# Performance work log

Hardware: AMD Instinct MI355X
Metric: run time of the kernel (lower is better)

The kernel has to match this reference:

```python
import jax, jax.numpy as jnp
import numpy as np

B, T, C, H = 4, 2048, 1024, 16
HS = C // H          # 64
DFF = 4 * C          # 4096
EPS = 1e-5


def _layernorm(x, g, b):
    mu = jnp.mean(x, axis=-1, keepdims=True)
    var = jnp.mean(jnp.square(x - mu), axis=-1, keepdims=True)
    return (x - mu) * jax.lax.rsqrt(var + EPS) * g + b


def setup_inputs() -> dict:
    key = jax.random.key(0)
    ks = jax.random.split(key, 12)
    s = 0.02
    return {
        "x": jax.random.normal(ks[0], (B, T, C), jnp.float32),
        "Wq": jax.random.normal(ks[1], (H, C, HS), jnp.float32) * s,
        "Wk": jax.random.normal(ks[2], (H, C, HS), jnp.float32) * s,
        "Wv": jax.random.normal(ks[3], (H, C, HS), jnp.float32) * s,
        "Wproj": jax.random.normal(ks[4], (C, C), jnp.float32) * s,
        "bproj": jnp.zeros((C,), jnp.float32),
        "ln1_g": jnp.ones((C,), jnp.float32),
        "ln1_b": jnp.zeros((C,), jnp.float32),
        "ln2_g": jnp.ones((C,), jnp.float32),
        "ln2_b": jnp.zeros((C,), jnp.float32),
        "W1": jax.random.normal(ks[5], (C, DFF), jnp.float32) * s,
        "b1": jnp.zeros((DFF,), jnp.float32),
        "W2": jax.random.normal(ks[6], (DFF, C), jnp.float32) * s,
        "b2": jnp.zeros((C,), jnp.float32),
    }


def reference(x, Wq, Wk, Wv, Wproj, bproj, ln1_g, ln1_b, ln2_g, ln2_b, W1, b1, W2, b2):
    Tn = x.shape[1]
    Cn = x.shape[2]
    # --- self-attention on ln1(x) ---
    h = _layernorm(x, ln1_g, ln1_b)
    q = jnp.einsum('btc,hcd->bhtd', h, Wq)
    k = jnp.einsum('btc,hcd->bhtd', h, Wk)
    v = jnp.einsum('btc,hcd->bhtd', h, Wv)
    # NOTE: original scales by C**-0.5 (full embed dim), not head_size**-0.5
    scores = jnp.einsum('bhtd,bhsd->bhts', q, k) * (Cn ** -0.5)
    mask = jnp.tril(jnp.ones((Tn, Tn), dtype=bool))
    scores = jnp.where(mask, scores, jnp.float32(-jnp.inf))
    att = jax.nn.softmax(scores, axis=-1)
    o = jnp.einsum('bhts,bhsd->bhtd', att, v)          # [B,H,T,HS]
    o = o.transpose(0, 2, 1, 3).reshape(x.shape)       # concat heads -> [B,T,C]
    x = x + o @ Wproj + bproj
    # --- feed-forward on ln2(x) ---
    h2 = _layernorm(x, ln2_g, ln2_b)
    x = x + jax.nn.relu(h2 @ W1 + b1) @ W2 + b2
    return x
```

## Files before the change

kernel.cpp:

```cpp
#include <hip/hip_runtime.h>
#include <hip/hip_bf16.h>
#include <stdint.h>

typedef __attribute__((ext_vector_type(8))) __bf16 bf16x8;
typedef __attribute__((ext_vector_type(4))) __bf16 bf16x4;
typedef __attribute__((ext_vector_type(4))) float f32x4;
typedef __attribute__((ext_vector_type(16))) float f32x16;
typedef __attribute__((ext_vector_type(4))) unsigned int u32x4;

typedef const __attribute__((address_space(1))) void* gas_ptr;
typedef __attribute__((address_space(3))) void* las_ptr;

static __device__ __forceinline__ void gload_lds16(const void* g, void* l) {
  __builtin_amdgcn_global_load_lds((gas_ptr)g, (las_ptr)l, 16, 0, 0);
}

static __device__ __forceinline__ unsigned int cvt_pk(float lo, float hi) {
  unsigned int r;
  asm("v_cvt_pk_bf16_f32 %0, %1, %2" : "=v"(r) : "v"(lo), "v"(hi));
  return r;
}

static __device__ __forceinline__ bf16x8 pack_frag(unsigned int a, unsigned int b,
                                                   unsigned int c, unsigned int d) {
  u32x4 t = {a, b, c, d};
  return __builtin_bit_cast(bf16x8, t);
}

static __device__ __forceinline__ void vm4() {
  asm volatile("s_waitcnt vmcnt(4)" ::: "memory");
}
static __device__ __forceinline__ void phase_bar() {
  asm volatile("" ::: "memory");
  __builtin_amdgcn_s_barrier();
  asm volatile("" ::: "memory");
}

__global__ void transpose_cvt(const float* __restrict__ in, __bf16* __restrict__ out,
                              int R, int S) {
  __shared__ float t[32][33];
  int tx = threadIdx.x, ty = threadIdx.y;
  int r0 = blockIdx.y * 32, s0 = blockIdx.x * 32;
#pragma unroll
  for (int i = 0; i < 4; ++i) {
    int r = r0 + ty + i * 8;
    if (r < R && (s0 + tx) < S) t[ty + i * 8][tx] = in[(size_t)r * S + s0 + tx];
  }
  __syncthreads();
#pragma unroll
  for (int i = 0; i < 4; ++i) {
    int s = s0 + ty + i * 8;
    if (s < S && (r0 + tx) < R) out[(size_t)s * R + r0 + tx] = (__bf16)t[tx][ty + i * 8];
  }
}

__global__ void qkv_repack(const float* __restrict__ Wq, const float* __restrict__ Wk,
                           const float* __restrict__ Wv, __bf16* __restrict__ outT) {
  __shared__ float t[32][33];
  int z = blockIdx.z, sel = z >> 4, h = z & 15;
  const float* in = (sel == 0 ? Wq : sel == 1 ? Wk : Wv) + (size_t)h * 1024 * 64;
  __bf16* out = outT + (size_t)(sel * 1024 + h * 64) * 1024;
  int tx = threadIdx.x, ty = threadIdx.y;
  int r0 = blockIdx.y * 32, s0 = blockIdx.x * 32;
#pragma unroll
  for (int i = 0; i < 4; ++i)
    t[ty + i * 8][tx] = in[(size_t)(r0 + ty + i * 8) * 64 + s0 + tx];
  __syncthreads();
#pragma unroll
  for (int i = 0; i < 4; ++i)
    out[(size_t)(s0 + ty + i * 8) * 1024 + r0 + tx] = (__bf16)t[tx][ty + i * 8];
}

__global__ __launch_bounds__(256) void ln_kernel(const float* __restrict__ x,
                                                 const float* __restrict__ g,
                                                 const float* __restrict__ b,
                                                 __bf16* __restrict__ out) {
  __shared__ float red[8];
  int row = blockIdx.x, tid = threadIdx.x;
  float4 v = ((const float4*)(x + (size_t)row * 1024))[tid];
  float s = v.x + v.y + v.z + v.w;
  float s2 = v.x * v.x + v.y * v.y + v.z * v.z + v.w * v.w;
#pragma unroll
  for (int m = 1; m < 64; m <<= 1) { s += __shfl_xor(s, m); s2 += __shfl_xor(s2, m); }
  if ((tid & 63) == 0) { red[tid >> 6] = s; red[4 + (tid >> 6)] = s2; }
  __syncthreads();
  s = red[0] + red[1] + red[2] + red[3];
  s2 = red[4] + red[5] + red[6] + red[7];
  float mu = s * (1.0f / 1024.0f);
  float var = s2 * (1.0f / 1024.0f) - mu * mu;
  float rs = rsqrtf(var + 1e-5f);
  float4 gg = ((const float4*)g)[tid];
  float4 bb = ((const float4*)b)[tid];
  bf16x4 o4;
  o4[0] = (__bf16)((v.x - mu) * rs * gg.x + bb.x);
  o4[1] = (__bf16)((v.y - mu) * rs * gg.y + bb.y);
  o4[2] = (__bf16)((v.z - mu) * rs * gg.z + bb.z);
  o4[3] = (__bf16)((v.w - mu) * rs * gg.w + bb.w);
  *(bf16x4*)(out + (size_t)row * 1024 + tid * 4) = o4;
}

__global__ __launch_bounds__(256) void add_bias_inplace(float* __restrict__ out,
                                                        const float* __restrict__ bias) {
  int i = blockIdx.x * 256 + threadIdx.x;
  float4 v = ((float4*)out)[i];
  float4 bb = ((const float4*)bias)[i & 255];
  v.x += bb.x; v.y += bb.y; v.z += bb.z; v.w += bb.w;
  ((float4*)out)[i] = v;
}

template <int EPI>
__global__ __launch_bounds__(512) void gemm8p(const __bf16* __restrict__ A,
                                              const __bf16* __restrict__ Bt,
                                              void* __restrict__ Cout,
                                              const float* __restrict__ bias,
                                              const float* __restrict__ resid,
                                              __bf16* __restrict__ q_out,
                                              __bf16* __restrict__ k_out,
                                              __bf16* __restrict__ vt_out,
                                              int M, int N, int K, int NBN) {
  __shared__ __align__(16) char lds[131072];
  const int tid = threadIdx.x;
  const int l = tid & 63, w = tid >> 6;
  const int wm = w >> 2, wn = w & 3;
  const int lr = l & 15, lg = l >> 4;

  int nwg = gridDim.x;
  int cpx = nwg >> 3;
  int orig = blockIdx.x;
  int wgid = (orig & 7) * cpx + (orig >> 3);
  int bn = wgid % NBN, bm = wgid / NBN;
  int n0 = bn * 256, m0 = bm * 256;

  const int Kloop = K / (int)gridDim.z;
  const int NT = Kloop >> 6;
  const size_t K2 = (size_t)K * 2;
  const size_t koff = (size_t)blockIdx.z * Kloop * 2;

  const int srow = tid >> 3, slot = tid & 7;
  const int sswz = (slot ^ (srow & 7)) << 4;
  const char* aA = (const char*)A + (size_t)(m0 + srow) * K2 + koff + sswz;
  const char* aB = (const char*)Bt + (size_t)(n0 + srow) * K2 + koff + sswz;

  auto stageA = [&](char* buf, int half, int kt) {
    char* d = buf + half * 16384 + tid * 16;
    const char* s = aA + (size_t)(half * 128) * K2 + (size_t)kt * 128;
    gload_lds16(s, d);
    gload_lds16(s + (size_t)64 * K2, d + 8192);
  };
  auto stageB = [&](char* buf, int half, int kt) {
    char* d = buf + 32768 + half * 16384 + tid * 16;
    const char* s = aB + (size_t)(half * 128) * K2 + (size_t)kt * 128;
    gload_lds16(s, d);
    gload_lds16(s + (size_t)64 * K2, d + 8192);
  };

  const int arow = (wm * 64 + lr) * 128;
  const int brow = (wn * 32 + lr) * 128;
  const int ck0 = ((lg) ^ (lr & 7)) << 4;
  const int ck1 = ((4 + lg) ^ (lr & 7)) << 4;

  f32x4 acc[8][4];
#pragma unroll
  for (int mi = 0; mi < 8; ++mi)
#pragma unroll
    for (int ni = 0; ni < 4; ++ni)
#pragma unroll
      for (int e = 0; e < 4; ++e) acc[mi][ni][e] = 0.0f;

  bf16x8 af[4][2], bfr[4][2];

  auto ldsA = [&](char* buf, int mh) {
#pragma unroll
    for (int i = 0; i < 4; ++i) {
      const char* p = buf + mh * 16384 + arow + i * 2048;
      af[i][0] = *(const bf16x8*)(p + ck0);
      af[i][1] = *(const bf16x8*)(p + ck1);
    }
  };
  auto ldsB2 = [&](char* buf, int nh) {
#pragma unroll
    for (int j = 0; j < 2; ++j) {
      const char* p = buf + 32768 + nh * 16384 + brow + j * 2048;
      bfr[nh * 2 + j][0] = *(const bf16x8*)(p + ck0);
      bfr[nh * 2 + j][1] = *(const bf16x8*)(p + ck1);
    }
  };
  auto mm = [&](int mh, int nh) {
    __builtin_amdgcn_s_setprio(1);
#pragma unroll
    for (int i = 0; i < 4; ++i)
#pragma unroll
      for (int j = 0; j < 2; ++j) {
        int mi = mh * 4 + i, ni = nh * 2 + j;
        acc[mi][ni] = __builtin_amdgcn_mfma_f32_16x16x32_bf16(af[i][0], bfr[ni][0], acc[mi][ni], 0, 0, 0);
        acc[mi][ni] = __builtin_amdgcn_mfma_f32_16x16x32_bf16(af[i][1], bfr[ni][1], acc[mi][ni], 0, 0, 0);
      }
    __builtin_amdgcn_s_setprio(0);
  };

  {
    char* b0 = lds;
    stageA(b0, 0, 0);
    stageB(b0, 0, 0);
    stageB(b0, 1, 0);
    stageA(b0, 1, 0);
  }

  for (int t = 0; t < NT; ++t) {
    char* cur = lds + ((t & 1) << 16);
    char* nxt = lds + (((t + 1) & 1) << 16);
    int kt = (t + 1 < NT) ? (t + 1) : (NT - 1);
    vm4();
    phase_bar();
    ldsA(cur, 0);
    ldsB2(cur, 0);
    stageA(nxt, 0, kt);
    mm(0, 0);
    vm4();
    phase_bar();
    ldsB2(cur, 1);
    stageB(nxt, 0, kt);
    mm(0, 1);
    vm4();
    phase_bar();
    ldsA(cur, 1);
    stageB(nxt, 1, kt);
    mm(1, 0);
    phase_bar();
    stageA(nxt, 1, kt);
    mm(1, 1);
  }

#pragma unroll
  for (int mi = 0; mi < 8; ++mi) {
    int rowb = m0 + (mi >> 2) * 128 + wm * 64 + (mi & 3) * 16 + lg * 4;
#pragma unroll
    for (int e = 0; e < 4; ++e) {
      int row = rowb + e;
#pragma unroll
      for (int ni = 0; ni < 4; ++ni) {
        int col = n0 + (ni >> 1) * 128 + wn * 32 + (ni & 1) * 16 + lr;
        float v = acc[mi][ni][e];
        size_t idx = (size_t)row * N + col;
        if (EPI == 0) {
          ((__bf16*)Cout)[idx] = (__bf16)v;
        } else if (EPI == 1) {
          ((float*)Cout)[idx] = resid[idx] + v + bias[col];
        } else if (EPI == 2) {
          v += bias[col];
          ((__bf16*)Cout)[idx] = (__bf16)fmaxf(v, 0.0f);
        } else if (EPI == 3) {
          unsafeAtomicAdd(&((float*)Cout)[idx], v);
        } else {
          int b = row >> 11, t = row & 2047;
          int sel = col >> 10, cc = col & 1023, h = cc >> 6, d = cc & 63;
          int bh = b * 16 + h;
          __bf16 val = (__bf16)v;
          if (sel == 0)
            q_out[((size_t)bh * 64 + d) * 2048 + t] = val;
          else if (sel == 1)
            k_out[((size_t)bh * 2048 + t) * 64 + d] = val;
          else
            vt_out[((size_t)bh * 64 + d) * 2048 + t] = val;
        }
      }
    }
  }
}

__global__ __launch_bounds__(256) void attn_kernel3(const __bf16* __restrict__ Qt,
                                                    const __bf16* __restrict__ Kh,
                                                    const __bf16* __restrict__ Vt,
                                                    __bf16* __restrict__ o) {
  __shared__ __align__(16) char Klds[8192];
  __shared__ __align__(16) char Vlds[8192];
  int tid = threadIdx.x;
  int l = tid & 63, w = tid >> 6;
  int lq = l & 31, hi = l >> 5;
  int p = blockIdx.x, bh = blockIdx.y;
  int b = bh >> 4, h = bh & 15;

  const char* Kbase = (const char*)(Kh + (size_t)bh * 2048 * 64);
  const char* Vbase = (const char*)(Vt + (size_t)bh * 64 * 2048);
  const __bf16* Qbase = Qt + (size_t)bh * 64 * 2048;
  __bf16* Obase = o + (size_t)b * 2048 * 1024 + h * 64;

  int srow = tid >> 3;
  int schunk = (tid & 7) * 16;
  int sw0 = (srow & 7) << 4;
  char* kd0 = Klds + tid * 16;
  char* kd1 = Klds + 4096 + tid * 16;
  char* vd0 = Vlds + tid * 16;
  char* vd1 = Vlds + 4096 + tid * 16;
  int swz = (lq & 7) << 4;

  for (int sweep = 0; sweep < 2; ++sweep) {
    int t = (sweep == 0) ? p : 15 - p;
    int qw = t * 128 + w * 32;
    int qglob = qw + lq;

    bf16x8 qb[4];
    const __bf16* qsrc = Qbase + (size_t)(hi * 8) * 2048 + qw + lq;
#pragma unroll
    for (int s = 0; s < 4; ++s)
#pragma unroll
      for (int j = 0; j < 8; ++j)
        qb[s][j] = qsrc[(size_t)(s * 16 + j) * 2048];

    f32x16 oacc0, oacc1;
#pragma unroll
    for (int i = 0; i < 16; ++i) { oacc0[i] = 0.0f; oacc1[i] = 0.0f; }
    float m_q = -3.0e38f, l_q = 0.0f;

    int nkb = 2 * t + 2;
    for (int kb = 0; kb < nkb; ++kb) {
      int s0 = kb * 64;
      __syncthreads();
      gload_lds16(Kbase + (size_t)(s0 + srow) * 128 + (schunk ^ sw0), kd0);
      gload_lds16(Kbase + (size_t)(s0 + srow + 32) * 128 + (schunk ^ sw0), kd1);
      gload_lds16(Vbase + (size_t)srow * 4096 + s0 * 2 + (schunk ^ sw0), vd0);
      gload_lds16(Vbase + (size_t)(srow + 32) * 4096 + s0 * 2 + (schunk ^ sw0), vd1);
      __syncthreads();

      f32x16 st0, st1;
#pragma unroll
      for (int i = 0; i < 16; ++i) { st0[i] = 0.0f; st1[i] = 0.0f; }
#pragma unroll
      for (int s = 0; s < 4; ++s) {
        bf16x8 ka = *(const bf16x8*)(Klds + lq * 128 + ((s * 32 + hi * 16) ^ swz));
        st0 = __builtin_amdgcn_mfma_f32_32x32x16_bf16(ka, qb[s], st0, 0, 0, 0);
      }
#pragma unroll
      for (int s = 0; s < 4; ++s) {
        bf16x8 ka = *(const bf16x8*)(Klds + (32 + lq) * 128 + ((s * 32 + hi * 16) ^ swz));
        st1 = __builtin_amdgcn_mfma_f32_32x32x16_bf16(ka, qb[s], st1, 0, 0, 0);
      }
#pragma unroll
      for (int r = 0; r < 16; ++r) {
        int key0 = s0 + (r & 3) + 8 * (r >> 2) + 4 * hi;
        if (key0 > qglob) st0[r] = -1.0e38f;
        if (key0 + 32 > qglob) st1[r] = -1.0e38f;
      }
      float mx8[8];
#pragma unroll
      for (int i = 0; i < 8; ++i)
        mx8[i] = fmaxf(fmaxf(st0[i], st0[i + 8]), fmaxf(st1[i], st1[i + 8]));
      float mx = fmaxf(fmaxf(fmaxf(mx8[0], mx8[1]), fmaxf(mx8[2], mx8[3])),
                       fmaxf(fmaxf(mx8[4], mx8[5]), fmaxf(mx8[6], mx8[7])));
      {
        float u = mx, v = mx;
        asm("v_permlane32_swap_b32 %0, %1" : "+v"(u), "+v"(v));
        mx = fmaxf(u, v);
      }
      float mt_s = mx * 0.03125f;
      if (__any(mt_s > m_q + 8.0f)) {
        float mnew = fmaxf(m_q, mt_s);
        float scv = exp2f((m_q - mnew) * 1.44269504f);
        m_q = mnew;
        l_q *= scv;
#pragma unroll
        for (int r = 0; r < 16; ++r) {
          int qr = (r & 3) + 8 * (r >> 2) + 4 * hi;
          float scO = __shfl(scv, qr);
          oacc0[r] *= scO;
          oacc1[r] *= scO;
        }
      }
      float m2 = m_q * 1.44269504f;
#pragma unroll
      for (int r = 0; r < 16; ++r) {
        st0[r] = exp2f(fmaf(st0[r], 0.045084389f, -m2));
        st1[r] = exp2f(fmaf(st1[r], 0.045084389f, -m2));
      }
      float s8[8];
#pragma unroll
      for (int i = 0; i < 8; ++i)
        s8[i] = (st0[i] + st0[i + 8]) + (st1[i] + st1[i + 8]);
      float ps = ((s8[0] + s8[1]) + (s8[2] + s8[3])) +
                 ((s8[4] + s8[5]) + (s8[6] + s8[7]));
      {
        float u = ps, v = ps;
        asm("v_permlane32_swap_b32 %0, %1" : "+v"(u), "+v"(v));
        ps = u + v;
      }
      l_q += ps;

      {
        unsigned int w0 = cvt_pk(st0[0], st0[1]), w1 = cvt_pk(st0[2], st0[3]);
        unsigned int w2 = cvt_pk(st0[4], st0[5]), w3 = cvt_pk(st0[6], st0[7]);
        asm("v_permlane32_swap_b32 %0, %1" : "+v"(w0), "+v"(w2));
        asm("v_permlane32_swap_b32 %0, %1" : "+v"(w1), "+v"(w3));
        bf16x8 pa0 = pack_frag(w0, w1, w2, w3);
        unsigned int w4 = cvt_pk(st0[8], st0[9]), w5 = cvt_pk(st0[10], st0[11]);
        unsigned int w6 = cvt_pk(st0[12], st0[13]), w7 = cvt_pk(st0[14], st0[15]);
        asm("v_permlane32_swap_b32 %0, %1" : "+v"(w4), "+v"(w6));
        asm("v_permlane32_swap_b32 %0, %1" : "+v"(w5), "+v"(w7));
        bf16x8 pa1 = pack_frag(w4, w5, w6, w7);
        bf16x8 v00 = *(const bf16x8*)(Vlds + lq * 128 + ((hi * 16) ^ swz));
        bf16x8 v01 = *(const bf16x8*)(Vlds + (32 + lq) * 128 + ((hi * 16) ^ swz));
        bf16x8 v10 = *(const bf16x8*)(Vlds + lq * 128 + ((32 + hi * 16) ^ swz));
        bf16x8 v11 = *(const bf16x8*)(Vlds + (32 + lq) * 128 + ((32 + hi * 16) ^ swz));
        oacc0 = __builtin_amdgcn_mfma_f32_32x32x16_bf16(pa0, v00, oacc0, 0, 0, 0);
        oacc1 = __builtin_amdgcn_mfma_f32_32x32x16_bf16(pa0, v01, oacc1, 0, 0, 0);
        oacc0 = __builtin_amdgcn_mfma_f32_32x32x16_bf16(pa1, v10, oacc0, 0, 0, 0);
        oacc1 = __builtin_amdgcn_mfma_f32_32x32x16_bf16(pa1, v11, oacc1, 0, 0, 0);
      }
      {
        unsigned int w0 = cvt_pk(st1[0], st1[1]), w1 = cvt_pk(st1[2], st1[3]);
        unsigned int w2 = cvt_pk(st1[4], st1[5]), w3 = cvt_pk(st1[6], st1[7]);
        asm("v_permlane32_swap_b32 %0, %1" : "+v"(w0), "+v"(w2));
        asm("v_permlane32_swap_b32 %0, %1" : "+v"(w1), "+v"(w3));
        bf16x8 pa0 = pack_frag(w0, w1, w2, w3);
        unsigned int w4 = cvt_pk(st1[8], st1[9]), w5 = cvt_pk(st1[10], st1[11]);
        unsigned int w6 = cvt_pk(st1[12], st1[13]), w7 = cvt_pk(st1[14], st1[15]);
        asm("v_permlane32_swap_b32 %0, %1" : "+v"(w4), "+v"(w6));
        asm("v_permlane32_swap_b32 %0, %1" : "+v"(w5), "+v"(w7));
        bf16x8 pa1 = pack_frag(w4, w5, w6, w7);
        bf16x8 v00 = *(const bf16x8*)(Vlds + lq * 128 + ((64 + hi * 16) ^ swz));
        bf16x8 v01 = *(const bf16x8*)(Vlds + (32 + lq) * 128 + ((64 + hi * 16) ^ swz));
        bf16x8 v10 = *(const bf16x8*)(Vlds + lq * 128 + ((96 + hi * 16) ^ swz));
        bf16x8 v11 = *(const bf16x8*)(Vlds + (32 + lq) * 128 + ((96 + hi * 16) ^ swz));
        oacc0 = __builtin_amdgcn_mfma_f32_32x32x16_bf16(pa0, v00, oacc0, 0, 0, 0);
        oacc1 = __builtin_amdgcn_mfma_f32_32x32x16_bf16(pa0, v01, oacc1, 0, 0, 0);
        oacc0 = __builtin_amdgcn_mfma_f32_32x32x16_bf16(pa1, v10, oacc0, 0, 0, 0);
        oacc1 = __builtin_amdgcn_mfma_f32_32x32x16_bf16(pa1, v11, oacc1, 0, 0, 0);
      }
    }
#pragma unroll
    for (int r = 0; r < 16; ++r) {
      int qr = (r & 3) + 8 * (r >> 2) + 4 * hi;
      float linv = 1.0f / __shfl(l_q, qr);
      size_t row = qw + qr;
      Obase[row * 1024 + lq] = (__bf16)(oacc0[r] * linv);
      Obase[row * 1024 + 32 + lq] = (__bf16)(oacc1[r] * linv);
    }
  }
}

extern "C" void kernel_launch(void* const* d_in, const int* in_sizes, int n_in,
                              void* d_out, int out_size, void* d_ws, size_t ws_size,
                              hipStream_t stream) {
  const float* x     = (const float*)d_in[0];
  const float* Wq    = (const float*)d_in[1];
  const float* Wk    = (const float*)d_in[2];
  const float* Wv    = (const float*)d_in[3];
  const float* Wproj = (const float*)d_in[4];
  const float* bproj = (const float*)d_in[5];
  const float* ln1_g = (const float*)d_in[6];
  const float* ln1_b = (const float*)d_in[7];
  const float* ln2_g = (const float*)d_in[8];
  const float* ln2_b = (const float*)d_in[9];
  const float* W1    = (const float*)d_in[10];
  const float* b1    = (const float*)d_in[11];
  const float* W2    = (const float*)d_in[12];
  const float* b2    = (const float*)d_in[13];
  float* out = (float*)d_out;

  char* ws = (char*)d_ws;
  __bf16* actA   = (__bf16*)(ws + 0);
  __bf16* WqkvT  = (__bf16*)(ws + 16777216);
  __bf16* WprojT = (__bf16*)(ws + 23068672);
  __bf16* W1T    = (__bf16*)(ws + 25165824);
  __bf16* W2T    = (__bf16*)(ws + 33554432);
  __bf16* Qt     = (__bf16*)(ws + 41943040);
  __bf16* Kh     = (__bf16*)(ws + 58720256);
  __bf16* Vt     = (__bf16*)(ws + 75497472);
  __bf16* obuf   = (__bf16*)(ws + 92274688);
  __bf16* ff1    = Qt;

  dim3 t32x8(32, 8);
  qkv_repack<<<dim3(2, 32, 48), t32x8, 0, stream>>>(Wq, Wk, Wv, WqkvT);
  transpose_cvt<<<dim3(32, 32), t32x8, 0, stream>>>(Wproj, WprojT, 1024, 1024);
  transpose_cvt<<<dim3(128, 32), t32x8, 0, stream>>>(W1, W1T, 1024, 4096);
  transpose_cvt<<<dim3(32, 128), t32x8, 0, stream>>>(W2, W2T, 4096, 1024);

  ln_kernel<<<8192, 256, 0, stream>>>(x, ln1_g, ln1_b, actA);
  gemm8p<4><<<dim3(384, 1, 1), 512, 0, stream>>>(actA, WqkvT, nullptr, nullptr, nullptr,
                                                 Qt, Kh, Vt, 8192, 3072, 1024, 12);
  attn_kernel3<<<dim3(8, 64), 256, 0, stream>>>(Qt, Kh, Vt, obuf);
  gemm8p<1><<<dim3(128, 1, 1), 512, 0, stream>>>(obuf, WprojT, out, bproj, x,
                                                 nullptr, nullptr, nullptr, 8192, 1024, 1024, 4);
  ln_kernel<<<8192, 256, 0, stream>>>(out, ln2_g, ln2_b, actA);
  add_bias_inplace<<<8192, 256, 0, stream>>>(out, b2);
  gemm8p<2><<<dim3(512, 1, 1), 512, 0, stream>>>(actA, W1T, ff1, b1, nullptr,
                                                 nullptr, nullptr, nullptr, 8192, 4096, 1024, 16);
  gemm8p<3><<<dim3(128, 1, 2), 512, 0, stream>>>(ff1, W2T, out, nullptr, nullptr,
                                                 nullptr, nullptr, nullptr, 8192, 1024, 4096, 4);
}
```

Measured before the change: 432.7 us.

## Deepen GEMM LDS pipeline and replace split-K atomics with bf16 partials plus reduce

The GEMM main loop is restructured into a two-tile unrolled schedule that prefetches one to two K-tiles ahead, reusing quarter-buffers of the current tile once they are consumed. It adds explicit lgkmcnt waits and sched barriers so LDS reads finish before the MFMAs. The split-K FF2 GEMM now writes two bf16 partial outputs instead of float atomics. A new reduce kernel sums the partials with the residual and b2, replacing the old bias-add kernel. Storing the partials in bf16 loses some precision, and the extra barriers per phase may add synchronization cost.

```diff
diff --git a/kernel.cpp b/kernel.cpp
--- a/kernel.cpp
+++ b/kernel.cpp
@@ -27,10 +27,17 @@
   return __builtin_bit_cast(bf16x8, t);
 }
 
-static __device__ __forceinline__ void vm4() {
-  asm volatile("s_waitcnt vmcnt(4)" ::: "memory");
-}
-static __device__ __forceinline__ void phase_bar() {
+static __device__ __forceinline__ void vm6() {
+  asm volatile("s_waitcnt vmcnt(6)" ::: "memory");
+}
+static __device__ __forceinline__ void vm8() {
+  asm volatile("s_waitcnt vmcnt(8)" ::: "memory");
+}
+static __device__ __forceinline__ void lgkm0sb() {
+  asm volatile("s_waitcnt lgkmcnt(0)" ::: "memory");
+  __builtin_amdgcn_sched_barrier(0);
+}
+static __device__ __forceinline__ void bar() {
   asm volatile("" ::: "memory");
   __builtin_amdgcn_s_barrier();
   asm volatile("" ::: "memory");
@@ -99,12 +106,19 @@
   *(bf16x4*)(out + (size_t)row * 1024 + tid * 4) = o4;
 }
 
-__global__ __launch_bounds__(256) void add_bias_inplace(float* __restrict__ out,
-                                                        const float* __restrict__ bias) {
+__global__ __launch_bounds__(256) void ff2_reduce(float* __restrict__ out,
+                                                  const __bf16* __restrict__ p0,
+                                                  const __bf16* __restrict__ p1,
+                                                  const float* __restrict__ b2) {
   int i = blockIdx.x * 256 + threadIdx.x;
-  float4 v = ((float4*)out)[i];
-  float4 bb = ((const float4*)bias)[i & 255];
-  v.x += bb.x; v.y += bb.y; v.z += bb.z; v.w += bb.w;
+  float4 v = ((const float4*)out)[i];
+  bf16x4 a = ((const bf16x4*)p0)[i];
+  bf16x4 b = ((const bf16x4*)p1)[i];
+  float4 bb = ((const float4*)b2)[i & 255];
+  v.x += (float)a[0] + (float)b[0] + bb.x;
+  v.y += (float)a[1] + (float)b[1] + bb.y;
+  v.z += (float)a[2] + (float)b[2] + bb.z;
+  v.w += (float)a[3] + (float)b[3] + bb.w;
   ((float4*)out)[i] = v;
 }
 
@@ -167,9 +181,9 @@
 #pragma unroll
       for (int e = 0; e < 4; ++e) acc[mi][ni][e] = 0.0f;
 
-  bf16x8 af[4][2], bfr[4][2];
-
-  auto ldsA = [&](char* buf, int mh) {
+  bf16x8 af[4][2], b0f[2][2], b1f[2][2];
+
+  auto ldsA = [&](const char* buf, int mh) {
 #pragma unroll
     for (int i = 0; i < 4; ++i) {
       const char* p = buf + mh * 16384 + arow + i * 2048;
@@ -177,58 +191,67 @@
       af[i][1] = *(const bf16x8*)(p + ck1);
     }
   };
-  auto ldsB2 = [&](char* buf, int nh) {
+  auto ldsB = [&](bf16x8 (&dst)[2][2], const char* buf, int nh) {
 #pragma unroll
     for (int j = 0; j < 2; ++j) {
       const char* p = buf + 32768 + nh * 16384 + brow + j * 2048;
-      bfr[nh * 2 + j][0] = *(const bf16x8*)(p + ck0);
-      bfr[nh * 2 + j][1] = *(const bf16x8*)(p + ck1);
+      dst[j][0] = *(const bf16x8*)(p + ck0);
+      dst[j][1] = *(const bf16x8*)(p + ck1);
     }
   };
-  auto mm = [&](int mh, int nh) {
+  auto mmq = [&](int mh, bf16x8 (&bf)[2][2], int nh) {
     __builtin_amdgcn_s_setprio(1);
 #pragma unroll
     for (int i = 0; i < 4; ++i)
 #pragma unroll
       for (int j = 0; j < 2; ++j) {
         int mi = mh * 4 + i, ni = nh * 2 + j;
-        acc[mi][ni] = __builtin_amdgcn_mfma_f32_16x16x32_bf16(af[i][0], bfr[ni][0], acc[mi][ni], 0, 0, 0);
-        acc[mi][ni] = __builtin_amdgcn_mfma_f32_16x16x32_bf16(af[i][1], bfr[ni][1], acc[mi][ni], 0, 0, 0);
+        acc[mi][ni] = __builtin_amdgcn_mfma_f32_16x16x32_bf16(af[i][0], bf[j][0], acc[mi][ni], 0, 0, 0);
+        acc[mi][ni] = __builtin_amdgcn_mfma_f32_16x16x32_bf16(af[i][1], bf[j][1], acc[mi][ni], 0, 0, 0);
       }
     __builtin_amdgcn_s_setprio(0);
   };
 
-  {
-    char* b0 = lds;
-    stageA(b0, 0, 0);
-    stageB(b0, 0, 0);
-    stageB(b0, 1, 0);
-    stageA(b0, 1, 0);
-  }
-
-  for (int t = 0; t < NT; ++t) {
-    char* cur = lds + ((t & 1) << 16);
-    char* nxt = lds + (((t + 1) & 1) << 16);
-    int kt = (t + 1 < NT) ? (t + 1) : (NT - 1);
-    vm4();
-    phase_bar();
+  char* bufE = lds;
+  char* bufO = lds + 65536;
+
+  stageA(bufE, 0, 0);
+  stageB(bufE, 0, 0);
+  stageB(bufE, 1, 0);
+  stageA(bufE, 1, 0);
+  if (NT > 1) { stageA(bufO, 0, 1); stageB(bufO, 0, 1); }
+  else        { stageA(bufO, 0, 0); stageB(bufO, 0, 0); }
+  vm8();
+  bar();
+
+  auto do_tile = [&](char* cur, char* oth, int t) {
+    int kN = (t + 1 < NT) ? t + 1 : NT - 1;
+    int kN2 = (t + 2 < NT) ? t + 2 : NT - 1;
     ldsA(cur, 0);
-    ldsB2(cur, 0);
-    stageA(nxt, 0, kt);
-    mm(0, 0);
-    vm4();
-    phase_bar();
-    ldsB2(cur, 1);
-    stageB(nxt, 0, kt);
-    mm(0, 1);
-    vm4();
-    phase_bar();
+    ldsB(b0f, cur, 0);
+    stageB(oth, 1, kN);
+    vm6(); bar(); lgkm0sb();
+    mmq(0, b0f, 0);
+    bar();
+    ldsB(b1f, cur, 1);
+    stageA(oth, 1, kN);
+    vm6(); bar(); lgkm0sb();
+    mmq(0, b1f, 1);
+    bar();
     ldsA(cur, 1);
-    stageB(nxt, 1, kt);
-    mm(1, 0);
-    phase_bar();
-    stageA(nxt, 1, kt);
-    mm(1, 1);
+    stageA(cur, 0, kN2);
+    vm6(); bar(); lgkm0sb();
+    mmq(1, b1f, 1);
+    bar();
+    stageB(cur, 0, kN2);
+    vm6(); bar();
+    mmq(1, b0f, 0);
+    bar();
+  };
+
+  for (int t = 0; t < NT; t += 2) {
+    do_tile(bufE, bufO, t);
+    do_tile(bufO, bufE, t + 1);
   }
 
 #pragma unroll
@@ -249,8 +272,8 @@
         } else if (EPI == 2) {
           v += bias[col];
           ((__bf16*)Cout)[idx] = (__bf16)fmaxf(v, 0.0f);
-        } else if (EPI == 3) {
-          unsafeAtomicAdd(&((float*)Cout)[idx], v);
+        } else if (EPI == 5) {
+          (blockIdx.z ? k_out : q_out)[idx] = (__bf16)v;
         } else {
           int b = row >> 11, t = row & 2047;
           int sel = col >> 10, cc = col & 1023, h = cc >> 6, d = cc & 63;
@@ -467,6 +490,8 @@
   __bf16* Vt     = (__bf16*)(ws + 75497472);
   __bf16* obuf   = (__bf16*)(ws + 92274688);
   __bf16* ff1    = Qt;
+  __bf16* p0     = (__bf16*)(ws + 0);
+  __bf16* p1     = (__bf16*)(ws + 16777216);
 
   dim3 t32x8(32, 8);
   qkv_repack<<<dim3(2, 32, 48), t32x8, 0, stream>>>(Wq, Wk, Wv, WqkvT);
@@ -481,9 +506,9 @@
   gemm8p<1><<<dim3(128, 1, 1), 512, 0, stream>>>(obuf, WprojT, out, bproj, x,
                                                  nullptr, nullptr, nullptr, 8192, 1024, 1024, 4);
   ln_kernel<<<8192, 256, 0, stream>>>(out, ln2_g, ln2_b, actA);
-  add_bias_inplace<<<8192, 256, 0, stream>>>(out, b2);
   gemm8p<2><<<dim3(512, 1, 1), 512, 0, stream>>>(actA, W1T, ff1, b1, nullptr,
                                                  nullptr, nullptr, nullptr, 8192, 4096, 1024, 16);
-  gemm8p<3><<<dim3(128, 1, 2), 512, 0, stream>>>(ff1, W2T, out, nullptr, nullptr,
-                                                 nullptr, nullptr, nullptr, 8192, 1024, 4096, 4);
-}
+  gemm8p<5><<<dim3(128, 1, 2), 512, 0, stream>>>(ff1, W2T, nullptr, nullptr, nullptr,
+                                                 p0, p1, nullptr, 8192, 1024, 4096, 4);
+  ff2_reduce<<<8192, 256, 0, stream>>>(out, p0, p1, b2);
+}
```

After: 404.3 us. 1.07x faster.
